# Performance work log

Hardware: AMD Instinct MI355X
Metric: run time of the kernel (lower is better)

## Reference

```python
import jax, jax.numpy as jnp
import numpy as np
from jax import lax

B, C, H, W = 4, 64, 128, 128
G, K, RED = 16, 7, 4        # groups, kernel size, reduce ratio
CR = C // RED               # reduced channels for kernel generation
EPS = 1e-5                  # BatchNorm eps (torch default)
DN = ('NCHW', 'OIHW', 'NCHW')


def setup_inputs() -> dict:
    key = jax.random.key(0)
    ks = jax.random.split(key, 5)
    return {
        'input': jax.random.normal(ks[0], (B, C, H, W), jnp.float32),
        # initial_mapping: depthwise 3x3 conv + pointwise 1x1 conv (bias=False)
        'w_dw': jax.random.normal(ks[1], (C, 1, 3, 3), jnp.float32) * 0.1,
        'w_pw': jax.random.normal(ks[2], (C, C), jnp.float32) * (1.0 / np.sqrt(C)),
        # sigma_mapping BatchNorm affine params
        'bn_gamma': jnp.ones((CR,), jnp.float32),
        'bn_beta': jnp.zeros((CR,), jnp.float32),
        # reduce / span 1x1 convs (bias=False)
        'w_reduce': jax.random.normal(ks[3], (CR, C), jnp.float32) * (1.0 / np.sqrt(C)),
        'w_span': jax.random.normal(ks[4], (K * K * G, CR), jnp.float32) * (1.0 / np.sqrt(CR)),
    }


def reference(input, w_dw, w_pw, bn_gamma, bn_beta, w_reduce, w_span):
    x = input
    # initial mapping: depthwise 3x3 (pad 1) then 1x1 pointwise
    h = lax.conv_general_dilated(x, w_dw, (1, 1), [(1, 1), (1, 1)],
                                 feature_group_count=C, dimension_numbers=DN)
    h = jnp.einsum('bchw,oc->bohw', h, w_pw)
    # unfold -> [B, C*K*K, H, W] with channel-major feature ordering (matches torch Unfold)
    patches = lax.conv_general_dilated_patches(h, (K, K), (1, 1), [(3, 3), (3, 3)],
                                               dimension_numbers=DN)
    patches = patches.reshape(B, G, C // G, K * K, H, W)
    # kernel generation: o_mapping is identity (stride 1 avg pool), then reduce -> BN(train) -> ReLU -> span
    r = jnp.einsum('bchw,oc->bohw', x, w_reduce)           # [B, CR, H, W]
    mean = r.mean(axis=(0, 2, 3), keepdims=True)
    var = r.var(axis=(0, 2, 3), keepdims=True)             # biased var, as torch BN training
    r = (r - mean) * lax.rsqrt(var + EPS) * bn_gamma[None, :, None, None] + bn_beta[None, :, None, None]
    r = jax.nn.relu(r)
    kern = jnp.einsum('bchw,oc->bohw', r, w_span)          # [B, G*K*K, H, W]
    kern = kern.reshape(B, G, 1, K * K, H, W)
    out = (kern * patches).sum(axis=3)                     # [B, G, C//G, H, W]
    return out.reshape(B, C, H, W)
```

## Files before the change

### kernel.cpp

```cpp
#include <hip/hip_runtime.h>

typedef _Float16 half2v __attribute__((ext_vector_type(2)));
typedef _Float16 half4v __attribute__((ext_vector_type(4)));
typedef _Float16 half8v __attribute__((ext_vector_type(8)));
typedef float f32x4 __attribute__((ext_vector_type(4)));

__launch_bounds__(256, 4)
__global__ void k_front(const float* __restrict__ in, const float* __restrict__ wdw,
                        const float* __restrict__ wpw, const float* __restrict__ wred,
                        _Float16* __restrict__ h16, _Float16* __restrict__ r16,
                        float* __restrict__ partial){
  __shared__ float4 s_in4[4][10][12];
  __shared__ __attribute__((aligned(16))) _Float16 s_dwh[64][72];
  __shared__ __attribute__((aligned(16))) _Float16 s_cvh[64][72];
  __shared__ float s_red[4][32];
  int t = threadIdx.x;
  int w = t >> 6, lane = t & 63;
  int lx = lane & 7, ly = lane >> 3;
  int c15 = lane & 15, hi = lane >> 4;
  int blk0 = blockIdx.x;

  int blk = ((blk0 & 7) << 7) | (blk0 >> 3);
  int tile = blk & 255, b = blk >> 8;
  int x0 = (tile & 15) << 3, y0 = (tile >> 4) << 3;
  const float* inb = in + ((long)b << 20) + ((long)(w << 2) << 14);

  const float* ap = wpw + (((w << 4) + c15) << 6) + (hi << 3);
  float4 ap0 = *(const float4*)(ap);
  float4 ap1 = *(const float4*)(ap + 4);
  float4 ap2 = *(const float4*)(ap + 32);
  float4 ap3 = *(const float4*)(ap + 36);
  const float* arp = wred + (c15 << 6) + (hi << 3);
  float4 ar0 = *(const float4*)(arp);
  float4 ar1 = *(const float4*)(arp + 4);
  float4 ar2 = *(const float4*)(arp + 32);
  float4 ar3 = *(const float4*)(arp + 36);
  half8v a_pw0 = {(_Float16)ap0.x,(_Float16)ap0.y,(_Float16)ap0.z,(_Float16)ap0.w,
                  (_Float16)ap1.x,(_Float16)ap1.y,(_Float16)ap1.z,(_Float16)ap1.w};
  half8v a_pw1 = {(_Float16)ap2.x,(_Float16)ap2.y,(_Float16)ap2.z,(_Float16)ap2.w,
                  (_Float16)ap3.x,(_Float16)ap3.y,(_Float16)ap3.z,(_Float16)ap3.w};
  half8v a_rd0 = {(_Float16)ar0.x,(_Float16)ar0.y,(_Float16)ar0.z,(_Float16)ar0.w,
                  (_Float16)ar1.x,(_Float16)ar1.y,(_Float16)ar1.z,(_Float16)ar1.w};
  half8v a_rd1 = {(_Float16)ar2.x,(_Float16)ar2.y,(_Float16)ar2.z,(_Float16)ar2.w,
                  (_Float16)ar3.x,(_Float16)ar3.y,(_Float16)ar3.z,(_Float16)ar3.w};

  int p1 = lane + 64;
  int ry0 = lane / 10, rx0 = lane - ry0 * 10;
  int ry1 = p1 / 10,   rx1 = p1 - ry1 * 10;
  int yy0 = y0 + ry0 - 1, xx0 = x0 + rx0 - 1;
  int yy1 = y0 + ry1 - 1, xx1 = x0 + rx1 - 1;
  bool ok0 = (unsigned)yy0 < 128u && (unsigned)xx0 < 128u;
  bool ok1 = (p1 < 100) && ((unsigned)yy1 < 128u) && ((unsigned)xx1 < 128u);
  int o0 = (yy0 << 7) + xx0, o1 = (yy1 << 7) + xx1;

  auto dw_dep = [&](int q){
    int wdbase = __builtin_amdgcn_readfirstlane(((q << 4) + (w << 2)) * 9);
    const float* wd = wdw + wdbase;
    float4 a = make_float4(0.f,0.f,0.f,0.f);
    float4 cv = make_float4(0.f,0.f,0.f,0.f);
    #pragma unroll
    for (int dy = 0; dy < 3; dy++){
      #pragma unroll
      for (int dx = 0; dx < 3; dx++){
        float4 v = s_in4[w][ly + dy][lx + dx];
        int k = dy * 3 + dx;
        a.x += v.x * wd[k];
        a.y += v.y * wd[9 + k];
        a.z += v.z * wd[18 + k];
        a.w += v.w * wd[27 + k];
        if (k == 4) cv = v;
      }
    }
    int cb = (q << 4) + (w << 2);
    half4v ah = {(_Float16)a.x,(_Float16)a.y,(_Float16)a.z,(_Float16)a.w};
    half4v eh = {(_Float16)cv.x,(_Float16)cv.y,(_Float16)cv.z,(_Float16)cv.w};
    *(half4v*)&s_dwh[lane][cb] = ah;
    *(half4v*)&s_cvh[lane][cb] = eh;
  };

  float4 vA0 = make_float4(0.f,0.f,0.f,0.f), vA1 = vA0, vB0 = vA0, vB1 = vA0;
  if (ok0){ vA0.x = inb[o0]; vA0.y = inb[o0+16384]; vA0.z = inb[o0+32768]; vA0.w = inb[o0+49152]; }
  if (ok1){ vA1.x = inb[o1]; vA1.y = inb[o1+16384]; vA1.z = inb[o1+32768]; vA1.w = inb[o1+49152]; }
  {
    const float* p1q = inb + (1L << 18);
    if (ok0){ vB0.x = p1q[o0]; vB0.y = p1q[o0+16384]; vB0.z = p1q[o0+32768]; vB0.w = p1q[o0+49152]; }
    if (ok1){ vB1.x = p1q[o1]; vB1.y = p1q[o1+16384]; vB1.z = p1q[o1+32768]; vB1.w = p1q[o1+49152]; }
  }

  #pragma unroll
  for (int qq = 0; qq < 2; qq++){
    s_in4[w][ry0][rx0] = vA0;
    if (p1 < 100) s_in4[w][ry1][rx1] = vA1;
    __builtin_amdgcn_wave_barrier();
    if (qq == 0){
      const float* pq = inb + (2L << 18);
      vA0 = make_float4(0.f,0.f,0.f,0.f); vA1 = vA0;
      if (ok0){ vA0.x = pq[o0]; vA0.y = pq[o0+16384]; vA0.z = pq[o0+32768]; vA0.w = pq[o0+49152]; }
      if (ok1){ vA1.x = pq[o1]; vA1.y = pq[o1+16384]; vA1.z = pq[o1+32768]; vA1.w = pq[o1+49152]; }
    }
    dw_dep(qq << 1);
    __builtin_amdgcn_wave_barrier();

    s_in4[w][ry0][rx0] = vB0;
    if (p1 < 100) s_in4[w][ry1][rx1] = vB1;
    __builtin_amdgcn_wave_barrier();
    if (qq == 0){
      const float* pq = inb + (3L << 18);
      vB0 = make_float4(0.f,0.f,0.f,0.f); vB1 = vB0;
      if (ok0){ vB0.x = pq[o0]; vB0.y = pq[o0+16384]; vB0.z = pq[o0+32768]; vB0.w = pq[o0+49152]; }
      if (ok1){ vB1.x = pq[o1]; vB1.y = pq[o1+16384]; vB1.z = pq[o1+32768]; vB1.w = pq[o1+49152]; }
    }
    dw_dep((qq << 1) + 1);
    __builtin_amdgcn_wave_barrier();
  }

  __syncthreads();

  f32x4 z = {0.f,0.f,0.f,0.f};
  f32x4 acc[4] = {z, z, z, z};
  #pragma unroll
  for (int tt = 0; tt < 4; tt++){
    half8v b0 = *(const half8v*)&s_dwh[(tt << 4) + c15][hi << 3];
    half8v b1 = *(const half8v*)&s_dwh[(tt << 4) + c15][32 + (hi << 3)];
    acc[tt] = __builtin_amdgcn_mfma_f32_16x16x32_f16(a_pw0, b0, acc[tt], 0, 0, 0);
    acc[tt] = __builtin_amdgcn_mfma_f32_16x16x32_f16(a_pw1, b1, acc[tt], 0, 0, 0);
  }
  #pragma unroll
  for (int tt = 0; tt < 4; tt++){
    int px = (tt << 4) + c15;
    int pyl = px >> 3, pxl = px & 7;
    int gout = (w << 2) + hi;
    long off = ((((long)((b << 4) + gout)) << 14) + ((y0 + pyl) << 7) + x0 + pxl) << 2;
    half4v hv = {(_Float16)acc[tt][0], (_Float16)acc[tt][1],
                 (_Float16)acc[tt][2], (_Float16)acc[tt][3]};
    *(half4v*)&h16[off] = hv;
  }

  f32x4 rac = z;
  {
    half8v b0 = *(const half8v*)&s_cvh[(w << 4) + c15][hi << 3];
    half8v b1 = *(const half8v*)&s_cvh[(w << 4) + c15][32 + (hi << 3)];
    rac = __builtin_amdgcn_mfma_f32_16x16x32_f16(a_rd0, b0, rac, 0, 0, 0);
    rac = __builtin_amdgcn_mfma_f32_16x16x32_f16(a_rd1, b1, rac, 0, 0, 0);
  }
  {
    int px = (w << 4) + c15;
    int pyl = px >> 3, pxl = px & 7;
    long roff = ((((long)b << 14) + ((y0 + pyl) << 7) + x0 + pxl) << 4) + (hi << 2);
    half4v rv4 = {(_Float16)rac[0], (_Float16)rac[1], (_Float16)rac[2], (_Float16)rac[3]};
    *(half4v*)&r16[roff] = rv4;
  }

  #pragma unroll
  for (int rr = 0; rr < 4; rr++){
    float v = rac[rr], s2 = v * v;
    #pragma unroll
    for (int m = 1; m < 16; m <<= 1){
      v  += __shfl_xor(v,  m, 64);
      s2 += __shfl_xor(s2, m, 64);
    }
    if (c15 == 0){
      int ch = (hi << 2) + rr;
      s_red[w][2 * ch]     = v;
      s_red[w][2 * ch + 1] = s2;
    }
  }
  __syncthreads();
  if (t < 32)
    partial[(blk0 << 5) + t] = s_red[0][t] + s_red[1][t] + s_red[2][t] + s_red[3][t];
}

__global__ void k_red(const float* __restrict__ partial, const float* __restrict__ gamma,
                      const float* __restrict__ beta, float* __restrict__ sb,
                      const float* __restrict__ wspan, _Float16* __restrict__ w16){
  __shared__ float sp[1024];
  int t = threadIdx.x;
  int c = t & 31, grp = t >> 5;
  float s = 0.f;
  #pragma unroll 4
  for (int i = grp; i < 1024; i += 32) s += partial[(i << 5) + c];
  sp[t] = s;
  for (int i = t; i < 12544; i += 1024) w16[i] = (_Float16)wspan[i];
  __syncthreads();
  if (t < 32){
    float v = 0.f;
    #pragma unroll
    for (int k = 0; k < 32; k++) v += sp[(k << 5) + t];
    sp[t] = v;
  }
  __syncthreads();
  if (t < 16){
    const float inv_n = 1.52587890625e-5f;
    float mean = sp[2 * t] * inv_n;
    float var  = sp[2 * t + 1] * inv_n - mean * mean;
    float inv  = rsqrtf(var + 1e-5f);
    float sc   = gamma[t] * inv;
    sb[2 * t]     = sc;
    sb[2 * t + 1] = beta[t] - mean * sc;
  }
}

__launch_bounds__(256)
__global__ void k_main(const _Float16* __restrict__ h16, const _Float16* __restrict__ r16,
                       const float* __restrict__ sb, const _Float16* __restrict__ w16,
                       float* __restrict__ out){
  __shared__ float4 s_h4[22][25];
  __shared__ float  s_sb[32];
  int t = threadIdx.x;
  int g = blockIdx.y, b = blockIdx.z;
  int bx = blockIdx.x;
  bx = ((bx & 7) << 3) | (bx >> 3);
  int tx0 = (bx & 7) << 4, ty0 = (bx >> 3) << 4;

  int ltx = t & 15, lty = t >> 4;
  int px = tx0 + ltx, py = ty0 + lty;

  const _Float16* rp = r16 + ((((long)b << 14) + (py << 7) + px) << 4);
  half8v ra = *(const half8v*)rp;
  half8v rb = *(const half8v*)(rp + 8);

  const _Float16* hp = h16 + (((long)((b << 4) + g)) << 16);
  for (int p = t; p < 484; p += 256){
    int ry = p / 22, rx = p - ry * 22;
    int yy = ty0 + ry - 3, xx = tx0 + rx - 3;
    float4 v = make_float4(0.f,0.f,0.f,0.f);
    if ((unsigned)yy < 128u && (unsigned)xx < 128u){
      half4v hh = *(const half4v*)&hp[(long)(((yy << 7) + xx) << 2)];
      v = make_float4((float)hh[0], (float)hh[1], (float)hh[2], (float)hh[3]);
    }
    s_h4[ry][rx] = v;
  }
  if (t < 32) s_sb[t] = sb[t];
  __syncthreads();

  float rv[16];
  #pragma unroll
  for (int c = 0; c < 8; c++){
    rv[c]     = fmaxf((float)ra[c] * s_sb[2*c]     + s_sb[2*c+1],     0.f);
    rv[c + 8] = fmaxf((float)rb[c] * s_sb[2*(c+8)] + s_sb[2*(c+8)+1], 0.f);
  }
#if __has_builtin(__builtin_amdgcn_fdot2)
  half2v rv2[8];
  #pragma unroll
  for (int j = 0; j < 8; j++){
    half2v pk; pk[0] = (_Float16)rv[2*j]; pk[1] = (_Float16)rv[2*j+1];
    rv2[j] = pk;
  }
#endif

  const _Float16* wg = w16 + g * 784;
#if __has_builtin(__builtin_amdgcn_fdot2)
  const half2v* wg2 = (const half2v*)wg;
#endif
  float acc0 = 0.f, acc1 = 0.f, acc2 = 0.f, acc3 = 0.f;
  #pragma unroll
  for (int kh = 0; kh < 7; kh++){
    #pragma unroll
    for (int kw = 0; kw < 7; kw++){
      int k = kh * 7 + kw;
      float kv0 = 0.f, kv1 = 0.f;
#if __has_builtin(__builtin_amdgcn_fdot2)
      #pragma unroll
      for (int j = 0; j < 4; j++){
        kv0 = __builtin_amdgcn_fdot2(rv2[j],     wg2[k*8 + j],     kv0, false);
        kv1 = __builtin_amdgcn_fdot2(rv2[j + 4], wg2[k*8 + j + 4], kv1, false);
      }
#else
      #pragma unroll
      for (int c = 0; c < 8; c++){
        kv0 += rv[c]     * (float)wg[k*16 + c];
        kv1 += rv[c + 8] * (float)wg[k*16 + c + 8];
      }
#endif
      float kv = kv0 + kv1;
      float4 hv = s_h4[lty + kh][ltx + kw];
      acc0 += kv * hv.x;
      acc1 += kv * hv.y;
      acc2 += kv * hv.z;
      acc3 += kv * hv.w;
    }
  }

  long obase = (((long)((b << 6) + (g << 2))) << 14) + (py << 7) + px;
  out[obase]         = acc0;
  out[obase + 16384] = acc1;
  out[obase + 32768] = acc2;
  out[obase + 49152] = acc3;
}

extern "C" void kernel_launch(void* const* d_in, const int* in_sizes, int n_in,
                              void* d_out, int out_size, void* d_ws, size_t ws_size,
                              hipStream_t stream){
  const float* in       = (const float*)d_in[0];
  const float* w_dw     = (const float*)d_in[1];
  const float* w_pw     = (const float*)d_in[2];
  const float* gamma    = (const float*)d_in[3];
  const float* beta     = (const float*)d_in[4];
  const float* w_reduce = (const float*)d_in[5];
  const float* w_span   = (const float*)d_in[6];
  float* out = (float*)d_out;

  _Float16* h16 = (_Float16*)d_ws;
  _Float16* r16 = h16 + 4194304;
  _Float16* w16 = r16 + 1048576;
  float* partial = (float*)(w16 + 16384);
  float* sb      = partial + 32768;

  k_front<<<1024, 256, 0, stream>>>(in, w_dw, w_pw, w_reduce, h16, r16, partial);
  k_red  <<<1, 1024, 0, stream>>>(partial, gamma, beta, sb, w_span, w16);
  dim3 grid(64, 16, 4);
  k_main <<<grid, 256, 0, stream>>>(h16, r16, sb, w16, out);
}
```

Measured before the change: 122.8 us.

## Replace LDS halo tile with direct per-thread global loads and row prefetch

k_main no longer stages the 22x22 halo tile of h into shared memory. Each thread instead loads its 7x7 neighbourhood straight from global memory (through the caches), double-buffering one row of seven half4 values ahead of the compute. The BN scale and bias are also read directly from global. This removes the shared-memory fill and the __syncthreads barrier. In exchange each input element is loaded up to 49 times across threads and register pressure rises.

```diff
diff --git a/kernel.cpp b/kernel.cpp
--- a/kernel.cpp
+++ b/kernel.cpp
@@ -204,8 +204,6 @@
 __global__ void k_main(const _Float16* __restrict__ h16, const _Float16* __restrict__ r16,
                        const float* __restrict__ sb, const _Float16* __restrict__ w16,
                        float* __restrict__ out){
-  __shared__ float4 s_h4[22][25];
-  __shared__ float  s_sb[32];
   int t = threadIdx.x;
   int g = blockIdx.y, b = blockIdx.z;
   int bx = blockIdx.x;
@@ -220,24 +218,28 @@
   half8v rb = *(const half8v*)(rp + 8);
 
   const _Float16* hp = h16 + (((long)((b << 4) + g)) << 16);
-  for (int p = t; p < 484; p += 256){
-    int ry = p / 22, rx = p - ry * 22;
-    int yy = ty0 + ry - 3, xx = tx0 + rx - 3;
-    float4 v = make_float4(0.f,0.f,0.f,0.f);
-    if ((unsigned)yy < 128u && (unsigned)xx < 128u){
-      half4v hh = *(const half4v*)&hp[(long)(((yy << 7) + xx) << 2)];
-      v = make_float4((float)hh[0], (float)hh[1], (float)hh[2], (float)hh[3]);
-    }
-    s_h4[ry][rx] = v;
-  }
-  if (t < 32) s_sb[t] = sb[t];
-  __syncthreads();
+
+  auto load_row = [&](int kh, half4v (&row)[7]){
+    int yy = py + kh - 3;
+    bool oky = (unsigned)yy < 128u;
+    const _Float16* hrow = hp + ((long)(yy << 7) << 2);
+    #pragma unroll
+    for (int kw = 0; kw < 7; kw++){
+      int xx = px + kw - 3;
+      half4v v = {0, 0, 0, 0};
+      if (oky && (unsigned)xx < 128u) v = *(const half4v*)&hrow[xx << 2];
+      row[kw] = v;
+    }
+  };
+
+  half4v cur[7], nxt[7];
+  load_row(0, cur);
 
   float rv[16];
   #pragma unroll
   for (int c = 0; c < 8; c++){
-    rv[c]     = fmaxf((float)ra[c] * s_sb[2*c]     + s_sb[2*c+1],     0.f);
-    rv[c + 8] = fmaxf((float)rb[c] * s_sb[2*(c+8)] + s_sb[2*(c+8)+1], 0.f);
+    rv[c]     = fmaxf((float)ra[c] * sb[2*c]     + sb[2*c+1],     0.f);
+    rv[c + 8] = fmaxf((float)rb[c] * sb[2*(c+8)] + sb[2*(c+8)+1], 0.f);
   }
 #if __has_builtin(__builtin_amdgcn_fdot2)
   half2v rv2[8];
@@ -255,6 +257,7 @@
   float acc0 = 0.f, acc1 = 0.f, acc2 = 0.f, acc3 = 0.f;
   #pragma unroll
   for (int kh = 0; kh < 7; kh++){
+    if (kh < 6) load_row(kh + 1, nxt);
     #pragma unroll
     for (int kw = 0; kw < 7; kw++){
       int k = kh * 7 + kw;
@@ -273,11 +276,15 @@
       }
 #endif
       float kv = kv0 + kv1;
-      float4 hv = s_h4[lty + kh][ltx + kw];
-      acc0 += kv * hv.x;
-      acc1 += kv * hv.y;
-      acc2 += kv * hv.z;
-      acc3 += kv * hv.w;
+      half4v hv = cur[kw];
+      acc0 += kv * (float)hv[0];
+      acc1 += kv * (float)hv[1];
+      acc2 += kv * (float)hv[2];
+      acc3 += kv * (float)hv[3];
+    }
+    if (kh < 6){
+      #pragma unroll
+      for (int j = 0; j < 7; j++) cur[j] = nxt[j];
     }
   }
 
```

After: 149.7 us. 1.22x slower.

## Compute generated kernel weights with MFMA instead of per-thread fdot2

Applied to the files above, without the earlier changes.

Each thread used to compute its 49 generated kernel values as 49 separate 16-channel fdot2 dot products. Now the ReLU'd reduced features are staged in LDS, and each wave computes a [64 pixels x 49 taps] product with 16x16x32 f16 MFMA instructions (K padded by zeroing the unused half). Results go into an LDS buffer s_kv that each thread then reads back into registers. w16 is zero-padded past 12544 elements so the MFMA A-tile reads past the last group stay in bounds. The aim is to cut VALU work in k_main. The cost is extra LDS traffic, about 53KB more shared memory, and 52 float registers per thread, which may lower occupancy.

```diff
diff --git a/kernel.cpp b/kernel.cpp
--- a/kernel.cpp
+++ b/kernel.cpp
@@ -181,6 +181,7 @@
   for (int i = grp; i < 1024; i += 32) s += partial[(i << 5) + c];
   sp[t] = s;
   for (int i = t; i < 12544; i += 1024) w16[i] = (_Float16)wspan[i];
+  for (int i = 12544 + t; i < 16384; i += 1024) w16[i] = (_Float16)0.f;
   __syncthreads();
   if (t < 32){
     float v = 0.f;
@@ -206,6 +207,8 @@
                        float* __restrict__ out){
   __shared__ float4 s_h4[22][25];
   __shared__ float  s_sb[32];
+  __shared__ __attribute__((aligned(16))) _Float16 s_rv[258][16];
+  __shared__ __attribute__((aligned(16))) float    s_kv[256][52];
   int t = threadIdx.x;
   int g = blockIdx.y, b = blockIdx.z;
   int bx = blockIdx.x;
@@ -214,6 +217,7 @@
 
   int ltx = t & 15, lty = t >> 4;
   int px = tx0 + ltx, py = ty0 + lty;
+  int lane = t & 63, w = t >> 6, c15 = lane & 15, hi = lane >> 4;
 
   const _Float16* rp = r16 + ((((long)b << 14) + (py << 7) + px) << 4);
   half8v ra = *(const half8v*)rp;
@@ -239,45 +243,49 @@
     rv[c]     = fmaxf((float)ra[c] * s_sb[2*c]     + s_sb[2*c+1],     0.f);
     rv[c + 8] = fmaxf((float)rb[c] * s_sb[2*(c+8)] + s_sb[2*(c+8)+1], 0.f);
   }
-#if __has_builtin(__builtin_amdgcn_fdot2)
-  half2v rv2[8];
-  #pragma unroll
-  for (int j = 0; j < 8; j++){
-    half2v pk; pk[0] = (_Float16)rv[2*j]; pk[1] = (_Float16)rv[2*j+1];
-    rv2[j] = pk;
-  }
-#endif
-
-  const _Float16* wg = w16 + g * 784;
-#if __has_builtin(__builtin_amdgcn_fdot2)
-  const half2v* wg2 = (const half2v*)wg;
-#endif
+  half8v rv_lo = {(_Float16)rv[0], (_Float16)rv[1], (_Float16)rv[2], (_Float16)rv[3],
+                  (_Float16)rv[4], (_Float16)rv[5], (_Float16)rv[6], (_Float16)rv[7]};
+  half8v rv_hi = {(_Float16)rv[8], (_Float16)rv[9], (_Float16)rv[10],(_Float16)rv[11],
+                  (_Float16)rv[12],(_Float16)rv[13],(_Float16)rv[14],(_Float16)rv[15]};
+  *(half8v*)&s_rv[t][0] = rv_lo;
+  *(half8v*)&s_rv[t][8] = rv_hi;
+  __builtin_amdgcn_wave_barrier();
+
+  const _Float16* wgg = w16 + g * 784;
+  f32x4 z = {0.f, 0.f, 0.f, 0.f};
+  int pbase = (w << 6) + c15;
+  int bco = (hi < 2) ? (hi << 3) : 0;
+  #pragma unroll
+  for (int rt = 0; rt < 4; rt++){
+    half8v a = {0,0,0,0,0,0,0,0};
+    if (hi < 2)
+      a = *(const half8v*)&wgg[(rt << 8) + (c15 << 4) + (hi << 3)];
+    #pragma unroll
+    for (int ct = 0; ct < 4; ct++){
+      half8v bf = *(const half8v*)&s_rv[pbase + (ct << 4)][bco];
+      f32x4 d = __builtin_amdgcn_mfma_f32_16x16x32_f16(a, bf, z, 0, 0, 0);
+      if (rt < 3 || hi == 0)
+        *(f32x4*)&s_kv[pbase + (ct << 4)][(rt << 4) + (hi << 2)] = d;
+    }
+  }
+  __builtin_amdgcn_wave_barrier();
+
+  float kv[52];
+  #pragma unroll
+  for (int j = 0; j < 13; j++)
+    *(f32x4*)&kv[j << 2] = *(const f32x4*)&s_kv[t][j << 2];
+
   float acc0 = 0.f, acc1 = 0.f, acc2 = 0.f, acc3 = 0.f;
   #pragma unroll
   for (int kh = 0; kh < 7; kh++){
     #pragma unroll
     for (int kw = 0; kw < 7; kw++){
-      int k = kh * 7 + kw;
-      float kv0 = 0.f, kv1 = 0.f;
-#if __has_builtin(__builtin_amdgcn_fdot2)
-      #pragma unroll
-      for (int j = 0; j < 4; j++){
-        kv0 = __builtin_amdgcn_fdot2(rv2[j],     wg2[k*8 + j],     kv0, false);
-        kv1 = __builtin_amdgcn_fdot2(rv2[j + 4], wg2[k*8 + j + 4], kv1, false);
-      }
-#else
-      #pragma unroll
-      for (int c = 0; c < 8; c++){
-        kv0 += rv[c]     * (float)wg[k*16 + c];
-        kv1 += rv[c + 8] * (float)wg[k*16 + c + 8];
-      }
-#endif
-      float kv = kv0 + kv1;
+      float kvv = kv[kh * 7 + kw];
       float4 hv = s_h4[lty + kh][ltx + kw];
-      acc0 += kv * hv.x;
-      acc1 += kv * hv.y;
-      acc2 += kv * hv.z;
-      acc3 += kv * hv.w;
+      acc0 += kvv * hv.x;
+      acc1 += kvv * hv.y;
+      acc2 += kvv * hv.z;
+      acc3 += kvv * hv.w;
     }
   }
 
```

New measurement: 129.4 us. 1.05x slower.
